# Kernel optimization log

Hardware: AMD Instinct MI355X
Metric: run time of the kernel (lower is better)

Reference implementation:

```python
import jax, jax.numpy as jnp
import numpy as np

P_BINS = 5
T_BINS = 16
B_BINS = P_BINS * T_BINS  # 80
IN_CH = 16
OUT_CH = 32
N_VERTS = 30000   # mesh vertices (cols of conn)
N_PATCH = 30000   # patches (rows of conn / B)
K_NNZ = 3         # nnz per sparse row (interpolation support)


def setup_inputs() -> dict:
    key = jax.random.key(0)
    k1, k2, k3, k4 = jax.random.split(key, 4)
    x = jax.random.normal(k1, (N_VERTS, IN_CH), dtype=jnp.float32)
    conn_idx = jax.random.randint(k2, (N_PATCH * B_BINS, K_NNZ), 0, N_VERTS, dtype=jnp.int32)
    conn_val = jax.random.uniform(k3, (N_PATCH * B_BINS, K_NNZ), dtype=jnp.float32)
    weights = jax.random.normal(k4, (B_BINS, IN_CH, OUT_CH), dtype=jnp.float32)
    return {"x": x, "conn_idx": conn_idx, "conn_val": conn_val, "weights": weights}


def _rotated_weights(weights):
    # layer_weights[j, :, :, i] = weights[(j + p*i) % B]  -> reshape (B*inp, out*t)
    j = jnp.arange(B_BINS)[:, None]
    i = jnp.arange(T_BINS)[None, :]
    idx = (j + P_BINS * i) % B_BINS                       # (B, t)
    lw = weights[idx]                                     # (B, t, inp, out)
    lw = jnp.transpose(lw, (0, 2, 3, 1))                  # (B, inp, out, t)
    return lw.reshape(B_BINS * IN_CH, OUT_CH * T_BINS)


def reference(x, conn_idx, conn_val, weights):
    # sparse.mm(conn, x): gather K vertex features per bin row and weight-sum
    gathered = jnp.einsum('rk,rkc->rc', conn_val, x[conn_idx])  # (N*B, inp)
    h = gathered.reshape(-1, B_BINS * IN_CH)                    # (N, B*inp)
    lw = _rotated_weights(weights)                              # (B*inp, out*t)
    y = h @ lw                                                  # (N, out*t)
    y = y.reshape(-1, OUT_CH, T_BINS)
    return jnp.max(y, axis=-1)                                  # (N, out)
```

## Files before the change

### kernel.cpp

```cpp
#include <hip/hip_runtime.h>
#include <hip/hip_bf16.h>
#include <stdint.h>

#define NP 30000
#define BBINS 80
#define INCH 16
#define OUTCH 32
#define KDIM 1280
#define NDIM 512
#define KSTEPS 40
#define NROWS (NP * BBINS)

typedef __bf16 bf16x8 __attribute__((ext_vector_type(8)));
typedef __bf16 bf16x4 __attribute__((ext_vector_type(4)));
typedef float f32x4 __attribute__((ext_vector_type(4)));

__device__ __forceinline__ void async_ld16(const void* g, void* l) {
    __builtin_amdgcn_global_load_lds(
        (const __attribute__((address_space(1))) unsigned int*)g,
        (__attribute__((address_space(3))) unsigned int*)l,
        16, 0, 0);
}

__global__ void prep_weights(const float* __restrict__ w, __bf16* __restrict__ pw) {
    int gid = blockIdx.x * 256 + threadIdx.x;
    int e  = gid & 7;
    int qs = (gid >> 3) & 3;
    int n  = (gid >> 5) & 511;
    int kc = gid >> 14;
    int kp = kc * 32 + ((qs ^ ((n >> 1) & 3)) << 3) + e;
    int b = kp >> 4, c = kp & 15;
    int o = n >> 4,  t = n & 15;
    int bid = (b + 5 * t) % BBINS;
    pw[gid] = (__bf16)w[(bid * INCH + c) * OUTCH + o];
}

__global__ __launch_bounds__(256) void gather_h(
    const float* __restrict__ x,
    const int*   __restrict__ cidx,
    const float* __restrict__ cval,
    __bf16* __restrict__ h) {
    __shared__ int   ci[192];
    __shared__ float cv[192];
    const int t  = threadIdx.x;
    const int r0 = blockIdx.x * 64;

    if (t < 48)
        ((int4*)ci)[t] = ((const int4*)(cidx + (size_t)r0 * 3))[t];
    else if (t >= 64 && t < 112)
        ((float4*)cv)[t - 64] = ((const float4*)(cval + (size_t)r0 * 3))[t - 64];
    __syncthreads();

    const int rl = t >> 2;
    const int q  = t & 3;
    const int i0 = ci[rl * 3 + 0], i1 = ci[rl * 3 + 1], i2 = ci[rl * 3 + 2];
    const float v0 = cv[rl * 3 + 0], v1 = cv[rl * 3 + 1], v2 = cv[rl * 3 + 2];

    const float4 a = *(const float4*)(x + (size_t)i0 * 16 + q * 4);
    const float4 b = *(const float4*)(x + (size_t)i1 * 16 + q * 4);
    const float4 c = *(const float4*)(x + (size_t)i2 * 16 + q * 4);
    bf16x4 hv;
    hv[0] = (__bf16)(v0 * a.x + v1 * b.x + v2 * c.x);
    hv[1] = (__bf16)(v0 * a.y + v1 * b.y + v2 * c.y);
    hv[2] = (__bf16)(v0 * a.z + v1 * b.z + v2 * c.z);
    hv[3] = (__bf16)(v0 * a.w + v1 * b.w + v2 * c.w);

    const int r   = r0 + rl;
    const int p   = r / 80;
    const int bin = r - p * 80;
    const int cl  = 2 * (bin & 1) + (q >> 1);
    const int slot = cl ^ ((p >> 1) & 3);
    const size_t off = (size_t)p * 2560 + (bin >> 1) * 64 + slot * 16 + (q & 1) * 8;
    *(bf16x4*)((char*)h + off) = hv;
}

__global__ __launch_bounds__(512, 2) void gemm_max(
    const __bf16* __restrict__ h,
    const __bf16* __restrict__ pw,
    float* __restrict__ out) {

    __shared__ __align__(16) char Abuf[2][16384];
    __shared__ __align__(16) char Bbuf[2][16384];

    const int m    = blockIdx.x >> 1;
    const int ncol = blockIdx.x & 1;
    const int mbase = m * 256;

    const int tid  = threadIdx.x;
    const int lane = tid & 63;
    const int wave = tid >> 6;
    const int wm = wave >> 1;
    const int wc = wave & 1;

    int a_off[4], b_off[8];
    {
        const int ml = lane & 15, q = lane >> 4;
        const int swz = (q ^ ((ml >> 1) & 3)) << 4;
#pragma unroll
        for (int i = 0; i < 4; ++i)
            a_off[i] = (wm * 64 + i * 16 + ml) * 64 + swz;
#pragma unroll
        for (int j = 0; j < 8; ++j)
            b_off[j] = (wc * 128 + j * 16 + ml) * 64 + swz;
    }

    f32x4 acc[4][8];
#pragma unroll
    for (int i = 0; i < 4; ++i)
#pragma unroll
        for (int j = 0; j < 8; ++j)
            acc[i][j] = (f32x4){0.f, 0.f, 0.f, 0.f};

    int rA0 = mbase + (tid >> 2);
    int rA1 = rA0 + 128;
    if (rA0 > NP - 1) rA0 = NP - 1;
    if (rA1 > NP - 1) rA1 = NP - 1;
    const char* aSrc0 = (const char*)h + (size_t)rA0 * 2560 + (tid & 3) * 16;
    const char* aSrc1 = (const char*)h + (size_t)rA1 * 2560 + (tid & 3) * 16;
    const char* bSrc  = (const char*)pw + ncol * 16384 + tid * 16;
    const int ldsOff  = tid * 16;

#define STAGE(KC, BUF)                                                  \
    do {                                                                \
        async_ld16(aSrc0 + (KC) * 64, Abuf[BUF] + ldsOff);              \
        async_ld16(aSrc1 + (KC) * 64, Abuf[BUF] + 8192 + ldsOff);       \
        async_ld16(bSrc + (KC) * 32768, Bbuf[BUF] + ldsOff);            \
        async_ld16(bSrc + (KC) * 32768 + 8192, Bbuf[BUF] + 8192 + ldsOff); \
    } while (0)

    STAGE(0, 0);

    for (int kc = 0; kc < KSTEPS; ++kc) {
        __syncthreads();
        if (kc + 1 < KSTEPS)
            STAGE(kc + 1, (kc + 1) & 1);

        const char* Ab = Abuf[kc & 1];
        const char* Bb = Bbuf[kc & 1];
        bf16x8 af[4], bfr[8];
#pragma unroll
        for (int i = 0; i < 4; ++i)
            af[i] = *(const bf16x8*)(Ab + a_off[i]);
#pragma unroll
        for (int j = 0; j < 8; ++j)
            bfr[j] = *(const bf16x8*)(Bb + b_off[j]);
#pragma unroll
        for (int i = 0; i < 4; ++i)
#pragma unroll
            for (int j = 0; j < 8; ++j)
                acc[i][j] = __builtin_amdgcn_mfma_f32_16x16x32_bf16(
                    af[i], bfr[j], acc[i][j], 0, 0, 0);
    }
#undef STAGE

    const int rgrp = lane >> 4;
    const int tl   = lane & 15;
#pragma unroll
    for (int i = 0; i < 4; ++i) {
#pragma unroll
        for (int j = 0; j < 8; ++j) {
            float v0 = acc[i][j][0], v1 = acc[i][j][1];
            float v2 = acc[i][j][2], v3 = acc[i][j][3];
#pragma unroll
            for (int off = 1; off < 16; off <<= 1) {
                v0 = fmaxf(v0, __shfl_xor(v0, off));
                v1 = fmaxf(v1, __shfl_xor(v1, off));
                v2 = fmaxf(v2, __shfl_xor(v2, off));
                v3 = fmaxf(v3, __shfl_xor(v3, off));
            }
            if (tl == 0) {
                const int o  = ncol * 16 + wc * 8 + j;
                const int pr = mbase + wm * 64 + i * 16 + rgrp * 4;
                if (pr + 0 < NP) out[(pr + 0) * 32 + o] = v0;
                if (pr + 1 < NP) out[(pr + 1) * 32 + o] = v1;
                if (pr + 2 < NP) out[(pr + 2) * 32 + o] = v2;
                if (pr + 3 < NP) out[(pr + 3) * 32 + o] = v3;
            }
        }
    }
}

extern "C" void kernel_launch(void* const* d_in, const int* in_sizes, int n_in,
                              void* d_out, int out_size, void* d_ws, size_t ws_size,
                              hipStream_t stream) {
    const float* x    = (const float*)d_in[0];
    const int*   cidx = (const int*)d_in[1];
    const float* cval = (const float*)d_in[2];
    const float* w    = (const float*)d_in[3];
    float* out = (float*)d_out;

    __bf16* pw = (__bf16*)d_ws;
    __bf16* h  = (__bf16*)((char*)d_ws + (2 << 20));

    hipLaunchKernelGGL(prep_weights, dim3(2560), dim3(256), 0, stream, w, pw);
    hipLaunchKernelGGL(gather_h, dim3(NROWS / 64), dim3(256), 0, stream,
                       x, cidx, cval, h);
    hipLaunchKernelGGL(gemm_max, dim3(((NP + 255) / 256) * 2), dim3(512), 0, stream,
                       h, (const __bf16*)pw, out);
}
```

Measured before the change: 209.9 us.

## Write h linearly in gather and swizzle A tiles via register-staged LDS stores

The gather kernel now writes each bf16 h row contiguously, dropping the per-row divide and XOR swizzle addressing, so its stores become simple coalesced writes. The GEMM instead loads A through registers with plain global loads and stores them into LDS at swizzled offsets after the MFMA work, while B keeps async global-to-LDS loads. The barrier moves to the end of each k-step. The grid is also remapped so blocks that share an M tile and differ in N column are spaced apart in launch order, with a padded grid and early exit. This trades some register pressure and VGPR-mediated stores in the GEMM for cheaper gather writes.

```diff
diff --git a/kernel.cpp b/kernel.cpp
--- a/kernel.cpp
+++ b/kernel.cpp
@@ -10,6 +10,7 @@
 #define NDIM 512
 #define KSTEPS 40
 #define NROWS (NP * BBINS)
+#define MTILES 118
 
 typedef __bf16 bf16x8 __attribute__((ext_vector_type(8)));
 typedef __bf16 bf16x4 __attribute__((ext_vector_type(4)));
@@ -65,13 +66,8 @@
     hv[2] = (__bf16)(v0 * a.z + v1 * b.z + v2 * c.z);
     hv[3] = (__bf16)(v0 * a.w + v1 * b.w + v2 * c.w);
 
-    const int r   = r0 + rl;
-    const int p   = r / 80;
-    const int bin = r - p * 80;
-    const int cl  = 2 * (bin & 1) + (q >> 1);
-    const int slot = cl ^ ((p >> 1) & 3);
-    const size_t off = (size_t)p * 2560 + (bin >> 1) * 64 + slot * 16 + (q & 1) * 8;
-    *(bf16x4*)((char*)h + off) = hv;
+    const int r = r0 + rl;
+    *(bf16x4*)((char*)h + (size_t)r * 32 + q * 8) = hv;
 }
 
 __global__ __launch_bounds__(512, 2) void gemm_max(
@@ -82,8 +78,10 @@
     __shared__ __align__(16) char Abuf[2][16384];
     __shared__ __align__(16) char Bbuf[2][16384];
 
-    const int m    = blockIdx.x >> 1;
-    const int ncol = blockIdx.x & 1;
+    const int bid = blockIdx.x;
+    const int m    = (bid >> 4) * 8 + (bid & 7);
+    const int ncol = (bid >> 3) & 1;
+    if (m >= MTILES) return;
     const int mbase = m * 256;
 
     const int tid  = threadIdx.x;
@@ -111,47 +109,62 @@
         for (int j = 0; j < 8; ++j)
             acc[i][j] = (f32x4){0.f, 0.f, 0.f, 0.f};
 
-    int rA0 = mbase + (tid >> 2);
-    int rA1 = rA0 + 128;
-    if (rA0 > NP - 1) rA0 = NP - 1;
-    if (rA1 > NP - 1) rA1 = NP - 1;
-    const char* aSrc0 = (const char*)h + (size_t)rA0 * 2560 + (tid & 3) * 16;
-    const char* aSrc1 = (const char*)h + (size_t)rA1 * 2560 + (tid & 3) * 16;
-    const char* bSrc  = (const char*)pw + ncol * 16384 + tid * 16;
-    const int ldsOff  = tid * 16;
-
-#define STAGE(KC, BUF)                                                  \
-    do {                                                                \
-        async_ld16(aSrc0 + (KC) * 64, Abuf[BUF] + ldsOff);              \
-        async_ld16(aSrc1 + (KC) * 64, Abuf[BUF] + 8192 + ldsOff);       \
-        async_ld16(bSrc + (KC) * 32768, Bbuf[BUF] + ldsOff);            \
-        async_ld16(bSrc + (KC) * 32768 + 8192, Bbuf[BUF] + 8192 + ldsOff); \
-    } while (0)
-
-    STAGE(0, 0);
+    const int aq = tid & 3;
+    int rL0 = (tid >> 2);
+    int rL1 = rL0 + 128;
+    int rG0 = mbase + rL0, rG1 = mbase + rL1;
+    if (rG0 > NP - 1) rG0 = NP - 1;
+    if (rG1 > NP - 1) rG1 = NP - 1;
+    const char* aSrc0 = (const char*)h + (size_t)rG0 * 2560 + aq * 16;
+    const char* aSrc1 = (const char*)h + (size_t)rG1 * 2560 + aq * 16;
+    const int aDst0 = rL0 * 64 + ((aq ^ ((rL0 >> 1) & 3)) << 4);
+    const int aDst1 = rL1 * 64 + ((aq ^ ((rL1 >> 1) & 3)) << 4);
+
+    const char* bSrc = (const char*)pw + ncol * 16384 + tid * 16;
+    const int ldsOff = tid * 16;
+
+    {
+        bf16x8 a0 = *(const bf16x8*)(aSrc0);
+        bf16x8 a1 = *(const bf16x8*)(aSrc1);
+        async_ld16(bSrc, Bbuf[0] + ldsOff);
+        async_ld16(bSrc + 8192, Bbuf[0] + 8192 + ldsOff);
+        *(bf16x8*)(Abuf[0] + aDst0) = a0;
+        *(bf16x8*)(Abuf[0] + aDst1) = a1;
+    }
+    __syncthreads();
 
     for (int kc = 0; kc < KSTEPS; ++kc) {
-        __syncthreads();
-        if (kc + 1 < KSTEPS)
-            STAGE(kc + 1, (kc + 1) & 1);
-
-        const char* Ab = Abuf[kc & 1];
-        const char* Bb = Bbuf[kc & 1];
+        const int cur = kc & 1, nxt = cur ^ 1;
+        bf16x8 a0, a1;
+        const bool more = (kc + 1 < KSTEPS);
+        if (more) {
+            a0 = *(const bf16x8*)(aSrc0 + (kc + 1) * 64);
+            a1 = *(const bf16x8*)(aSrc1 + (kc + 1) * 64);
+            const char* bs = bSrc + (size_t)(kc + 1) * 32768;
+            async_ld16(bs, Bbuf[nxt] + ldsOff);
+            async_ld16(bs + 8192, Bbuf[nxt] + 8192 + ldsOff);
+        }
+
         bf16x8 af[4], bfr[8];
 #pragma unroll
         for (int i = 0; i < 4; ++i)
-            af[i] = *(const bf16x8*)(Ab + a_off[i]);
+            af[i] = *(const bf16x8*)(Abuf[cur] + a_off[i]);
 #pragma unroll
         for (int j = 0; j < 8; ++j)
-            bfr[j] = *(const bf16x8*)(Bb + b_off[j]);
+            bfr[j] = *(const bf16x8*)(Bbuf[cur] + b_off[j]);
 #pragma unroll
         for (int i = 0; i < 4; ++i)
 #pragma unroll
             for (int j = 0; j < 8; ++j)
                 acc[i][j] = __builtin_amdgcn_mfma_f32_16x16x32_bf16(
                     af[i], bfr[j], acc[i][j], 0, 0, 0);
-    }
-#undef STAGE
+
+        if (more) {
+            *(bf16x8*)(Abuf[nxt] + aDst0) = a0;
+            *(bf16x8*)(Abuf[nxt] + aDst1) = a1;
+        }
+        __syncthreads();
+    }
 
     const int rgrp = lane >> 4;
     const int tl   = lane & 15;
@@ -195,6 +208,6 @@
     hipLaunchKernelGGL(prep_weights, dim3(2560), dim3(256), 0, stream, w, pw);
     hipLaunchKernelGGL(gather_h, dim3(NROWS / 64), dim3(256), 0, stream,
                        x, cidx, cval, h);
-    hipLaunchKernelGGL(gemm_max, dim3(((NP + 255) / 256) * 2), dim3(512), 0, stream,
+    hipLaunchKernelGGL(gemm_max, dim3(240), dim3(512), 0, stream,
                        h, (const __bf16*)pw, out);
 }
```

New measurement: 198.5 us. 1.06x faster.

## Triple-buffer GEMM staging, fuse weight prep into gather, remap tiles

Applied to the files above, without the earlier changes.

The GEMM now keeps three LDS buffers and prefetches two K-steps ahead. It synchronises with explicit vmcnt waits plus s_barrier instead of a __syncthreads at the top of every step, so more global-to-LDS latency is hidden. The weight-permutation kernel is folded into the gather kernel as extra blocks, saving one launch. GEMM blocks are also remapped so groups of 8 M-tiles share a column half, with a fixed 240-block grid and early exit for out-of-range tiles. The larger LDS footprint of about 96KB per block may limit the declared two blocks per CU.

```diff
diff --git a/kernel.cpp b/kernel.cpp
--- a/kernel.cpp
+++ b/kernel.cpp
@@ -10,6 +10,8 @@
 #define NDIM 512
 #define KSTEPS 40
 #define NROWS (NP * BBINS)
+#define MTILES 118
+#define PREP_BLOCKS 2560
 
 typedef __bf16 bf16x8 __attribute__((ext_vector_type(8)));
 typedef __bf16 bf16x4 __attribute__((ext_vector_type(4)));
@@ -22,28 +24,32 @@
         16, 0, 0);
 }
 
-__global__ void prep_weights(const float* __restrict__ w, __bf16* __restrict__ pw) {
-    int gid = blockIdx.x * 256 + threadIdx.x;
-    int e  = gid & 7;
-    int qs = (gid >> 3) & 3;
-    int n  = (gid >> 5) & 511;
-    int kc = gid >> 14;
-    int kp = kc * 32 + ((qs ^ ((n >> 1) & 3)) << 3) + e;
-    int b = kp >> 4, c = kp & 15;
-    int o = n >> 4,  t = n & 15;
-    int bid = (b + 5 * t) % BBINS;
-    pw[gid] = (__bf16)w[(bid * INCH + c) * OUTCH + o];
-}
-
-__global__ __launch_bounds__(256) void gather_h(
+__global__ __launch_bounds__(256) void prep_gather(
     const float* __restrict__ x,
     const int*   __restrict__ cidx,
     const float* __restrict__ cval,
+    const float* __restrict__ w,
+    __bf16* __restrict__ pw,
     __bf16* __restrict__ h) {
     __shared__ int   ci[192];
     __shared__ float cv[192];
+
+    if (blockIdx.x < PREP_BLOCKS) {
+        int gid = blockIdx.x * 256 + threadIdx.x;
+        int e  = gid & 7;
+        int qs = (gid >> 3) & 3;
+        int n  = (gid >> 5) & 511;
+        int kc = gid >> 14;
+        int kp = kc * 32 + ((qs ^ ((n >> 1) & 3)) << 3) + e;
+        int b = kp >> 4, c = kp & 15;
+        int o = n >> 4,  t = n & 15;
+        int bid = (b + 5 * t) % BBINS;
+        pw[gid] = (__bf16)w[(bid * INCH + c) * OUTCH + o];
+        return;
+    }
+
     const int t  = threadIdx.x;
-    const int r0 = blockIdx.x * 64;
+    const int r0 = (blockIdx.x - PREP_BLOCKS) * 64;
 
     if (t < 48)
         ((int4*)ci)[t] = ((const int4*)(cidx + (size_t)r0 * 3))[t];
@@ -68,7 +74,7 @@
     const int r   = r0 + rl;
     const int p   = r / 80;
     const int bin = r - p * 80;
-    const int cl  = 2 * (bin & 1) + (q >> 1);
+    const int cl   = 2 * (bin & 1) + (q >> 1);
     const int slot = cl ^ ((p >> 1) & 3);
     const size_t off = (size_t)p * 2560 + (bin >> 1) * 64 + slot * 16 + (q & 1) * 8;
     *(bf16x4*)((char*)h + off) = hv;
@@ -79,11 +85,13 @@
     const __bf16* __restrict__ pw,
     float* __restrict__ out) {
 
-    __shared__ __align__(16) char Abuf[2][16384];
-    __shared__ __align__(16) char Bbuf[2][16384];
-
-    const int m    = blockIdx.x >> 1;
-    const int ncol = blockIdx.x & 1;
+    __shared__ __align__(16) char Abuf[3][16384];
+    __shared__ __align__(16) char Bbuf[3][16384];
+
+    const int bid = blockIdx.x;
+    const int m    = (bid >> 4) * 8 + (bid & 7);
+    const int ncol = (bid >> 3) & 1;
+    if (m >= MTILES) return;
     const int mbase = m * 256;
 
     const int tid  = threadIdx.x;
@@ -111,47 +119,55 @@
         for (int j = 0; j < 8; ++j)
             acc[i][j] = (f32x4){0.f, 0.f, 0.f, 0.f};
 
-    int rA0 = mbase + (tid >> 2);
-    int rA1 = rA0 + 128;
-    if (rA0 > NP - 1) rA0 = NP - 1;
-    if (rA1 > NP - 1) rA1 = NP - 1;
-    const char* aSrc0 = (const char*)h + (size_t)rA0 * 2560 + (tid & 3) * 16;
-    const char* aSrc1 = (const char*)h + (size_t)rA1 * 2560 + (tid & 3) * 16;
+    const int aq = tid & 3;
+    int rG0 = mbase + (tid >> 2);
+    int rG1 = rG0 + 128;
+    if (rG0 > NP - 1) rG0 = NP - 1;
+    if (rG1 > NP - 1) rG1 = NP - 1;
+    const char* aSrc0 = (const char*)h + (size_t)rG0 * 2560 + aq * 16;
+    const char* aSrc1 = (const char*)h + (size_t)rG1 * 2560 + aq * 16;
     const char* bSrc  = (const char*)pw + ncol * 16384 + tid * 16;
     const int ldsOff  = tid * 16;
 
-#define STAGE(KC, BUF)                                                  \
-    do {                                                                \
-        async_ld16(aSrc0 + (KC) * 64, Abuf[BUF] + ldsOff);              \
-        async_ld16(aSrc1 + (KC) * 64, Abuf[BUF] + 8192 + ldsOff);       \
-        async_ld16(bSrc + (KC) * 32768, Bbuf[BUF] + ldsOff);            \
-        async_ld16(bSrc + (KC) * 32768 + 8192, Bbuf[BUF] + 8192 + ldsOff); \
+#define STAGE(KC, BUF)                                                   \
+    do {                                                                 \
+        async_ld16(aSrc0 + (KC) * 64, Abuf[BUF] + ldsOff);               \
+        async_ld16(aSrc1 + (KC) * 64, Abuf[BUF] + 8192 + ldsOff);        \
+        async_ld16(bSrc + (size_t)(KC) * 32768, Bbuf[BUF] + ldsOff);     \
+        async_ld16(bSrc + (size_t)(KC) * 32768 + 8192,                   \
+                   Bbuf[BUF] + 8192 + ldsOff);                           \
     } while (0)
 
+#define WAITB(N) asm volatile("s_waitcnt vmcnt(" #N ")\n\ts_barrier" ::: "memory")
+
     STAGE(0, 0);
+    STAGE(1, 1);
+    WAITB(4);
 
     for (int kc = 0; kc < KSTEPS; ++kc) {
-        __syncthreads();
-        if (kc + 1 < KSTEPS)
-            STAGE(kc + 1, (kc + 1) & 1);
-
-        const char* Ab = Abuf[kc & 1];
-        const char* Bb = Bbuf[kc & 1];
+        const int cur = kc % 3;
+        if (kc + 2 < KSTEPS)
+            STAGE(kc + 2, (kc + 2) % 3);
+
         bf16x8 af[4], bfr[8];
 #pragma unroll
         for (int i = 0; i < 4; ++i)
-            af[i] = *(const bf16x8*)(Ab + a_off[i]);
+            af[i] = *(const bf16x8*)(Abuf[cur] + a_off[i]);
 #pragma unroll
         for (int j = 0; j < 8; ++j)
-            bfr[j] = *(const bf16x8*)(Bb + b_off[j]);
+            bfr[j] = *(const bf16x8*)(Bbuf[cur] + b_off[j]);
 #pragma unroll
         for (int i = 0; i < 4; ++i)
 #pragma unroll
             for (int j = 0; j < 8; ++j)
                 acc[i][j] = __builtin_amdgcn_mfma_f32_16x16x32_bf16(
                     af[i], bfr[j], acc[i][j], 0, 0, 0);
+
+        if (kc + 2 < KSTEPS)      WAITB(4);
+        else if (kc + 1 < KSTEPS) WAITB(0);
     }
 #undef STAGE
+#undef WAITB
 
     const int rgrp = lane >> 4;
     const int tl   = lane & 15;
@@ -192,9 +208,8 @@
     __bf16* pw = (__bf16*)d_ws;
     __bf16* h  = (__bf16*)((char*)d_ws + (2 << 20));
 
-    hipLaunchKernelGGL(prep_weights, dim3(2560), dim3(256), 0, stream, w, pw);
-    hipLaunchKernelGGL(gather_h, dim3(NROWS / 64), dim3(256), 0, stream,
-                       x, cidx, cval, h);
-    hipLaunchKernelGGL(gemm_max, dim3(((NP + 255) / 256) * 2), dim3(512), 0, stream,
+    hipLaunchKernelGGL(prep_gather, dim3(PREP_BLOCKS + NROWS / 64), dim3(256), 0,
+                       stream, x, cidx, cval, w, pw, h);
+    hipLaunchKernelGGL(gemm_max, dim3(240), dim3(512), 0, stream,
                        h, (const __bf16*)pw, out);
 }
```

After: 202.4 us. -3.5%, faster.
